# Kernel tuning notes

Measured on AMD Instinct MI355X. Metric: run time of the kernel, lower is better.

The kernel has to match this reference:

```python
import jax, jax.numpy as jnp
import numpy as np

K = 5            # kernel_size
MAX_ORIENT = 8
MAX_LEVEL = 4
D = (K - 1) // 2  # pad amount = 2


def setup_inputs() -> dict:
    key = jax.random.key(0)
    k1, k2, k3 = jax.random.split(key, 3)
    x = jax.random.normal(k1, (32, 1, 512, 512), dtype=jnp.float32)
    fwd_f = jax.random.normal(k2, (MAX_ORIENT, 1, K, K), dtype=jnp.float32)
    fwd_f = fwd_f.at[0, 0].set(jnp.ones((K, K), dtype=jnp.float32))  # per __init__
    inv_f = jax.random.normal(k3, (MAX_ORIENT, 1, K, K), dtype=jnp.float32)
    return {"x": x, "forward_filters": fwd_f, "inverse_filters": inv_f}


def _pad_for_tconv(p):
    # faithful port of padding_for_transpose_conv (static python ints)
    ip, op = 0, 0
    if p > 0:
        op = p
    elif p < 0:
        a = -p
        if a % 2 == 0:
            ip = a // 2
        else:
            op = 1
            ip = (a + 1) // 2
    return ip, op


def _conv2d(x, w, stride, pad):
    # torch F.pad(x, (d,d,d,d)) then conv2d(stride) == conv with symmetric padding
    return jax.lax.conv_general_dilated(
        x, w, window_strides=(stride, stride),
        padding=((pad, pad), (pad, pad)),
        dimension_numbers=("NCHW", "OIHW", "NCHW"))


def _conv_transpose2d(x, w, stride, pad, out_pad):
    # torch conv_transpose2d, weight layout (in_ch, out_ch, kH, kW).
    # Equivalent direct conv: flip kernel spatially, swap I/O axes,
    # lhs_dilation=stride, padding lo=k-1-p, hi=k-1-p+output_padding.
    k = w.shape[2]
    w2 = jnp.transpose(jnp.flip(w, (2, 3)), (1, 0, 2, 3))  # OIHW (1,8,5,5)
    padding = tuple((k - 1 - p, k - 1 - p + op) for p, op in zip(pad, out_pad))
    return jax.lax.conv_general_dilated(
        x, w2, window_strides=(1, 1), padding=padding,
        lhs_dilation=(stride, stride),
        dimension_numbers=("NCHW", "OIHW", "NCHW"))


def _forward_transform(x, fwd_f):
    result = [None] * (MAX_LEVEL + 1)
    vimg = x
    level = MAX_LEVEL
    res = None
    while level > 0 and vimg.shape[2] > 1 and vimg.shape[3] > 1:
        res = _conv2d(vimg, fwd_f, 2, D)   # (B, 8, ceil(H/2)+?, ...)
        result[level] = res
        vimg = res[:, :1]                  # lowpass band feeds next level
        level -= 1
    result[0] = res[:, :1]
    return result


def _inverse_transform(coeffs, inp_dim, inv_f):
    rec = coeffs[0]
    for level in range(1, MAX_LEVEL + 1):
        cur = np.array(coeffs[level].shape[2:])
        target = np.array(inp_dim) if level == MAX_LEVEL else np.array(coeffs[level + 1].shape[2:])
        pc = target - 2 * (cur - 1) - K
        ip0, op0 = _pad_for_tconv(int(pc[0]))
        ip1, op1 = _pad_for_tconv(int(pc[1]))
        full = jnp.concatenate([rec, coeffs[level][:, 1:]], axis=1)  # (B,8,h,w)
        rec = _conv_transpose2d(full, inv_f, 2, (ip0, ip1), (op0, op1))
    return rec


def reference(x, forward_filters, inverse_filters):
    coeffs = _forward_transform(x, forward_filters)
    return _inverse_transform(coeffs, x.shape[2:], inverse_filters)
```

## Files before the change

### kernel.cpp

```cpp
#include <hip/hip_runtime.h>

#define NORIENT 8

__device__ __forceinline__ unsigned xcd_swz(unsigned bid, unsigned nwg) {
    unsigned chunk = nwg >> 3;
    return (nwg & 7u) ? bid : (bid & 7u) * chunk + (bid >> 3);
}

__global__ void fwd_conv_wave_kernel(const float* __restrict__ in, long in_img_stride,
                                     const float* __restrict__ filt,
                                     float* __restrict__ out,
                                     int H, int W, int OH, int OW, int N) {
    constexpr int SROW = 104;
    __shared__ float tile[67 * SROW];

    int nbx = OW >> 5, nby = OH >> 5;
    unsigned sb = xcd_swz(blockIdx.x, gridDim.x);
    int bx = (int)(sb % nbx);
    unsigned t = sb / nbx;
    int by = (int)(t % nby);
    int n = (int)(t / nby);

    const float* __restrict__ ip = in + (long)n * in_img_stride;
    int tid = threadIdx.x;

    int w = __builtin_amdgcn_readfirstlane(tid >> 6);
    const float* __restrict__ F = filt + w * 25;
    float Wt[25];
#pragma unroll
    for (int k = 0; k < 25; ++k) Wt[k] = F[k];

    int gy0 = 64 * by - 2, gx0 = 64 * bx - 4;
#pragma unroll
    for (int k = 0; k < 3; ++k) {
        int e = tid + k * 512;
        if (e < 67 * 18) {
            int row = e / 18, m = e - row * 18;
            int gy = gy0 + row, gx = gx0 + 4 * m;
            bool vl = (gy >= 0) & (gy < H) & (gx >= 0) & (gx <= W - 4);
            float4 val = *(const float4*)(ip + (vl ? ((long)gy * W + gx) : 0));
            float msk = vl ? 1.f : 0.f;
            int off = row * SROW + 4 * m + 4 * (m >> 1);
            *(float4*)&tile[off] = make_float4(val.x * msk, val.y * msk,
                                               val.z * msk, val.w * msk);
        }
    }
    __syncthreads();

    int lane = tid & 63;
    int lx = lane & 7, ly = lane >> 3;

    float acc[4][4];
#pragma unroll
    for (int o = 0; o < 4; ++o)
#pragma unroll
        for (int dx = 0; dx < 4; ++dx) acc[o][dx] = 0.f;

#pragma unroll
    for (int r = 0; r < 11; ++r) {
        int base = (8 * ly + r) * SROW + 12 * lx;
        float4 A = *(const float4*)&tile[base];
        float4 B = *(const float4*)&tile[base + 4];
        float4 C = *(const float4*)&tile[base + 12];
        float4 Dd = *(const float4*)&tile[base + 16];
        float P[16] = {A.x, A.y, A.z, A.w, B.x, B.y, B.z, B.w,
                       C.x, C.y, C.z, C.w, Dd.x, Dd.y, Dd.z, Dd.w};

#pragma unroll
        for (int o = 0; o < 4; ++o) {
            int i = r - 2 * o;
            if (i < 0 || i > 4) continue;
#pragma unroll
            for (int j = 0; j < 5; ++j) {
                float wv = Wt[i * 5 + j];
#pragma unroll
                for (int dx = 0; dx < 4; ++dx)
                    acc[o][dx] = fmaf(P[2 + 2 * dx + j], wv, acc[o][dx]);
            }
        }
    }

    long cs = (long)OH * OW;
    int oy = 32 * by + 4 * ly, ox = 32 * bx + 4 * lx;
    long ob = ((long)n * NORIENT + w) * cs + (long)oy * OW + ox;
#pragma unroll
    for (int o = 0; o < 4; ++o)
        *(float4*)(out + ob + (long)o * OW) =
            make_float4(acc[o][0], acc[o][1], acc[o][2], acc[o][3]);
}

__global__ void inv_tconv_kernel(const float* __restrict__ rec, long rec_img_stride,
                                 const float* __restrict__ coef,
                                 const float* __restrict__ filt,
                                 float* __restrict__ out,
                                 int h, int w, int N) {
    int h2 = h >> 1, w2 = w >> 1;
    unsigned sb = xcd_swz(blockIdx.x, gridDim.x);
    long idx = (long)sb * blockDim.x + threadIdx.x;
    long total = (long)N * h2 * w2;
    if (idx >= total) return;
    int b0 = (int)(idx % w2);
    long t = idx / w2;
    int a0 = (int)(t % h2);
    int n = (int)(t / h2);

    const float* __restrict__ rp = rec + (long)n * rec_img_stride;
    const float* __restrict__ cp = coef + (long)n * (long)NORIENT * h * w;
    int cs = h * w;

    bool fmv = a0 > 0, fpv = a0 < h2 - 1;
    bool um = b0 > 0, up = b0 < w2 - 1;
    float fm = fmv ? 1.f : 0.f, fp_ = fpv ? 1.f : 0.f;
    int r0 = (fmv ? 2 * a0 - 1 : 0) * w;
    int r1 = (2 * a0) * w;
    int r2 = (2 * a0 + 1) * w;
    int r3 = (fpv ? 2 * a0 + 2 : 2 * a0 + 1) * w;
    int cL = um ? 2 * b0 - 2 : 0;
    int cM = 2 * b0;
    int cR = up ? 2 * b0 + 2 : 0;

    float acc[2][2][2][2];
#pragma unroll
    for (int i = 0; i < 2; ++i)
#pragma unroll
        for (int j = 0; j < 2; ++j)
#pragma unroll
            for (int k = 0; k < 2; ++k)
#pragma unroll
                for (int l = 0; l < 2; ++l) acc[i][j][k][l] = 0.f;

    auto do_channel = [&](const float* __restrict__ src, const float* __restrict__ F) {
        float P[4][4];
        const int ro[4] = {r0, r1, r2, r3};
        const float rm[4] = {fm, 1.f, 1.f, fp_};
#pragma unroll
        for (int r = 0; r < 4; ++r) {
            const float* base = src + ro[r];
            float2 L = *(const float2*)(base + cL);
            float2 M = *(const float2*)(base + cM);
            float2 R = *(const float2*)(base + cR);
            float mask = rm[r];
            P[r][0] = (um ? L.y : 0.f) * mask;
            P[r][1] = M.x * mask;
            P[r][2] = M.y * mask;
            P[r][3] = (up ? R.x : 0.f) * mask;
        }
#pragma unroll
        for (int a = 0; a < 3; ++a) {
#pragma unroll
            for (int b = 0; b < 3; ++b) {
                float w00 = F[(4 - 2 * a) * 5 + (4 - 2 * b)];
                float w01 = (b >= 1) ? F[(4 - 2 * a) * 5 + (5 - 2 * b)] : 0.f;
                float w10 = (a >= 1) ? F[(5 - 2 * a) * 5 + (4 - 2 * b)] : 0.f;
                float w11 = (a >= 1 && b >= 1) ? F[(5 - 2 * a) * 5 + (5 - 2 * b)] : 0.f;
#pragma unroll
                for (int sr = 0; sr < 2; ++sr) {
#pragma unroll
                    for (int sc = 0; sc < 2; ++sc) {
                        float pv = P[sr + a][sc + b];
                        acc[sr][sc][0][0] = fmaf(pv, w00, acc[sr][sc][0][0]);
                        if (b >= 1) acc[sr][sc][0][1] = fmaf(pv, w01, acc[sr][sc][0][1]);
                        if (a >= 1) acc[sr][sc][1][0] = fmaf(pv, w10, acc[sr][sc][1][0]);
                        if (a >= 1 && b >= 1)
                                    acc[sr][sc][1][1] = fmaf(pv, w11, acc[sr][sc][1][1]);
                    }
                }
            }
        }
    };

    do_channel(rp, filt);
#pragma unroll
    for (int c = 1; c < NORIENT; ++c)
        do_channel(cp + (long)c * cs, filt + c * 25);

    int OW = w << 1;
    long ob = (long)n * 4 * (long)cs + (long)(4 * a0) * OW + 4 * b0;
    *(float4*)(out + ob)          = make_float4(acc[0][0][0][0], acc[0][0][0][1],
                                                acc[0][1][0][0], acc[0][1][0][1]);
    *(float4*)(out + ob + OW)     = make_float4(acc[0][0][1][0], acc[0][0][1][1],
                                                acc[0][1][1][0], acc[0][1][1][1]);
    *(float4*)(out + ob + 2 * OW) = make_float4(acc[1][0][0][0], acc[1][0][0][1],
                                                acc[1][1][0][0], acc[1][1][0][1]);
    *(float4*)(out + ob + 3 * OW) = make_float4(acc[1][0][1][0], acc[1][0][1][1],
                                                acc[1][1][1][0], acc[1][1][1][1]);
}

extern "C" void kernel_launch(void* const* d_in, const int* in_sizes, int n_in,
                              void* d_out, int out_size, void* d_ws, size_t ws_size,
                              hipStream_t stream) {
    const float* x     = (const float*)d_in[0];
    const float* fwd_f = (const float*)d_in[1];
    const float* inv_f = (const float*)d_in[2];
    float* out = (float*)d_out;
    float* ws  = (float*)d_ws;

    const int N = 32;

    float* l4 = ws;
    float* l3 = l4 + 16777216;
    float* l2 = l3 + 4194304;
    float* l1 = l2 + 1048576;
    float* r1 = l1 + 262144;
    float* r2 = r1 + 131072;
    float* r3 = r2 + 524288;

    dim3 blkF(512), blk(256);
    auto nblocks = [](long total) { return dim3((unsigned)((total + 255) / 256)); };

    fwd_conv_wave_kernel<<<dim3(32 * 8 * 8), blkF, 0, stream>>>(
        x, 512L * 512, fwd_f, l4, 512, 512, 256, 256, N);
    fwd_conv_wave_kernel<<<dim3(32 * 4 * 4), blkF, 0, stream>>>(
        l4, 8L * 256 * 256, fwd_f, l3, 256, 256, 128, 128, N);
    fwd_conv_wave_kernel<<<dim3(32 * 2 * 2), blkF, 0, stream>>>(
        l3, 8L * 128 * 128, fwd_f, l2, 128, 128, 64, 64, N);
    fwd_conv_wave_kernel<<<dim3(32 * 1 * 1), blkF, 0, stream>>>(
        l2, 8L * 64 * 64, fwd_f, l1, 64, 64, 32, 32, N);

    inv_tconv_kernel<<<nblocks(32L * 16 * 16), blk, 0, stream>>>(
        l1, 8L * 32 * 32, l1, inv_f, r1, 32, 32, N);
    inv_tconv_kernel<<<nblocks(32L * 32 * 32), blk, 0, stream>>>(
        r1, 64L * 64, l2, inv_f, r2, 64, 64, N);
    inv_tconv_kernel<<<nblocks(32L * 64 * 64), blk, 0, stream>>>(
        r2, 128L * 128, l3, inv_f, r3, 128, 128, N);
    inv_tconv_kernel<<<nblocks(32L * 128 * 128), blk, 0, stream>>>(
        r3, 256L * 256, l4, inv_f, out, 256, 256, N);
}
```

Before: 96.53 us.

## Stage inverse transposed-conv input tiles in LDS for all eight channels

The inverse transposed-convolution kernel now assigns each 256-thread block a 32x32 input tile, loads a haloed 34x40 patch of all eight channel planes into shared memory with float4 loads, and computes from LDS. Previously each thread did overlapping global float2 loads with per-thread boundary logic. The aim is to remove redundant global and cache traffic and the masking arithmetic, at the cost of a large LDS footprint (about 43 KB per block), which may limit occupancy.

```diff
diff --git a/kernel.cpp b/kernel.cpp
--- a/kernel.cpp
+++ b/kernel.cpp
@@ -89,35 +89,78 @@
             make_float4(acc[o][0], acc[o][1], acc[o][2], acc[o][3]);
 }
 
-__global__ void inv_tconv_kernel(const float* __restrict__ rec, long rec_img_stride,
-                                 const float* __restrict__ coef,
-                                 const float* __restrict__ filt,
-                                 float* __restrict__ out,
-                                 int h, int w, int N) {
-    int h2 = h >> 1, w2 = w >> 1;
+__global__ void inv_tconv_lds_kernel(const float* __restrict__ rec, long rec_img_stride,
+                                     const float* __restrict__ coef,
+                                     const float* __restrict__ filt,
+                                     float* __restrict__ out,
+                                     int h, int w, int N) {
+    constexpr int SROW = 40;
+    constexpr int CH = 34 * SROW;
+    __shared__ float tile[NORIENT * CH];
+
+    int nbx = w >> 5, nby = h >> 5;
     unsigned sb = xcd_swz(blockIdx.x, gridDim.x);
-    long idx = (long)sb * blockDim.x + threadIdx.x;
-    long total = (long)N * h2 * w2;
-    if (idx >= total) return;
-    int b0 = (int)(idx % w2);
-    long t = idx / w2;
-    int a0 = (int)(t % h2);
-    int n = (int)(t / h2);
-
+    int bx = (int)(sb % nbx);
+    unsigned tt = sb / nbx;
+    int by = (int)(tt % nby);
+    int n = (int)(tt / nby);
+
+    int S0 = 32 * by, Q0 = 32 * bx;
+    long cs = (long)h * w;
     const float* __restrict__ rp = rec + (long)n * rec_img_stride;
-    const float* __restrict__ cp = coef + (long)n * (long)NORIENT * h * w;
-    int cs = h * w;
-
-    bool fmv = a0 > 0, fpv = a0 < h2 - 1;
-    bool um = b0 > 0, up = b0 < w2 - 1;
-    float fm = fmv ? 1.f : 0.f, fp_ = fpv ? 1.f : 0.f;
-    int r0 = (fmv ? 2 * a0 - 1 : 0) * w;
-    int r1 = (2 * a0) * w;
-    int r2 = (2 * a0 + 1) * w;
-    int r3 = (fpv ? 2 * a0 + 2 : 2 * a0 + 1) * w;
-    int cL = um ? 2 * b0 - 2 : 0;
-    int cM = 2 * b0;
-    int cR = up ? 2 * b0 + 2 : 0;
+    const float* __restrict__ cp = coef + (long)n * NORIENT * cs;
+
+    int tid = threadIdx.x;
+
+    {
+        float4 v[6]; int o[6]; unsigned msk = 0;
+#pragma unroll
+        for (int k = 0; k < 6; ++k) {
+            int e = tid + 256 * k;
+            int ech = e / 340, rem = e - ech * 340;
+            int row = rem / 10, m = rem - row * 10;
+            int gy = S0 - 1 + row, gx = Q0 - 4 + 4 * m;
+            bool vl = (gy >= 0) & (gy < h) & (gx >= 0) & (gx <= w - 4);
+            const float* __restrict__ src = ech ? (cp + (long)ech * cs) : rp;
+            v[k] = *(const float4*)(src + (vl ? ((long)gy * w + gx) : 0));
+            o[k] = ech * CH + row * SROW + 4 * m;
+            msk |= (vl ? 1u : 0u) << k;
+        }
+#pragma unroll
+        for (int k = 0; k < 6; ++k) {
+            float mm = ((msk >> k) & 1u) ? 1.f : 0.f;
+            *(float4*)&tile[o[k]] = make_float4(v[k].x * mm, v[k].y * mm,
+                                                v[k].z * mm, v[k].w * mm);
+        }
+    }
+    {
+        float4 v[5]; int o[5]; unsigned msk = 0;
+#pragma unroll
+        for (int k = 0; k < 5; ++k) {
+            int e = tid + 256 * (6 + k);
+            bool inr = e < 2720;
+            int e2 = inr ? e : 0;
+            int ech = e2 / 340, rem = e2 - ech * 340;
+            int row = rem / 10, m = rem - row * 10;
+            int gy = S0 - 1 + row, gx = Q0 - 4 + 4 * m;
+            bool vl = inr & (gy >= 0) & (gy < h) & (gx >= 0) & (gx <= w - 4);
+            const float* __restrict__ src = ech ? (cp + (long)ech * cs) : rp;
+            v[k] = *(const float4*)(src + (vl ? ((long)gy * w + gx) : 0));
+            o[k] = inr ? (ech * CH + row * SROW + 4 * m) : -1;
+            msk |= (vl ? 1u : 0u) << k;
+        }
+#pragma unroll
+        for (int k = 0; k < 5; ++k) {
+            if (o[k] >= 0) {
+                float mm = ((msk >> k) & 1u) ? 1.f : 0.f;
+                *(float4*)&tile[o[k]] = make_float4(v[k].x * mm, v[k].y * mm,
+                                                    v[k].z * mm, v[k].w * mm);
+            }
+        }
+    }
+    __syncthreads();
+
+    int sx = tid & 15, sy = tid >> 4;
 
     float acc[2][2][2][2];
 #pragma unroll
@@ -129,22 +172,20 @@
 #pragma unroll
                 for (int l = 0; l < 2; ++l) acc[i][j][k][l] = 0.f;
 
-    auto do_channel = [&](const float* __restrict__ src, const float* __restrict__ F) {
+#pragma unroll
+    for (int c = 0; c < NORIENT; ++c) {
+        const float* __restrict__ F = filt + c * 25;
+        const float* __restrict__ tc = &tile[c * CH];
+
         float P[4][4];
-        const int ro[4] = {r0, r1, r2, r3};
-        const float rm[4] = {fm, 1.f, 1.f, fp_};
 #pragma unroll
         for (int r = 0; r < 4; ++r) {
-            const float* base = src + ro[r];
-            float2 L = *(const float2*)(base + cL);
-            float2 M = *(const float2*)(base + cM);
-            float2 R = *(const float2*)(base + cR);
-            float mask = rm[r];
-            P[r][0] = (um ? L.y : 0.f) * mask;
-            P[r][1] = M.x * mask;
-            P[r][2] = M.y * mask;
-            P[r][3] = (up ? R.x : 0.f) * mask;
-        }
+            const float* rowp = tc + (2 * sy + r) * SROW;
+            float2 L = *(const float2*)(rowp + 2 * sx + 2);
+            float4 Ff = *(const float4*)(rowp + 2 * sx + 4);
+            P[r][0] = L.y; P[r][1] = Ff.x; P[r][2] = Ff.y; P[r][3] = Ff.z;
+        }
+
 #pragma unroll
         for (int a = 0; a < 3; ++a) {
 #pragma unroll
@@ -167,15 +208,10 @@
                 }
             }
         }
-    };
-
-    do_channel(rp, filt);
-#pragma unroll
-    for (int c = 1; c < NORIENT; ++c)
-        do_channel(cp + (long)c * cs, filt + c * 25);
+    }
 
     int OW = w << 1;
-    long ob = (long)n * 4 * (long)cs + (long)(4 * a0) * OW + 4 * b0;
+    long ob = (long)n * 4 * cs + (long)(2 * S0 + 4 * sy) * OW + (2 * Q0 + 4 * sx);
     *(float4*)(out + ob)          = make_float4(acc[0][0][0][0], acc[0][0][0][1],
                                                 acc[0][1][0][0], acc[0][1][0][1]);
     *(float4*)(out + ob + OW)     = make_float4(acc[0][0][1][0], acc[0][0][1][1],
@@ -206,7 +242,6 @@
     float* r3 = r2 + 524288;
 
     dim3 blkF(512), blk(256);
-    auto nblocks = [](long total) { return dim3((unsigned)((total + 255) / 256)); };
 
     fwd_conv_wave_kernel<<<dim3(32 * 8 * 8), blkF, 0, stream>>>(
         x, 512L * 512, fwd_f, l4, 512, 512, 256, 256, N);
@@ -217,12 +252,12 @@
     fwd_conv_wave_kernel<<<dim3(32 * 1 * 1), blkF, 0, stream>>>(
         l2, 8L * 64 * 64, fwd_f, l1, 64, 64, 32, 32, N);
 
-    inv_tconv_kernel<<<nblocks(32L * 16 * 16), blk, 0, stream>>>(
+    inv_tconv_lds_kernel<<<dim3(32 * 1 * 1), blk, 0, stream>>>(
         l1, 8L * 32 * 32, l1, inv_f, r1, 32, 32, N);
-    inv_tconv_kernel<<<nblocks(32L * 32 * 32), blk, 0, stream>>>(
+    inv_tconv_lds_kernel<<<dim3(32 * 2 * 2), blk, 0, stream>>>(
         r1, 64L * 64, l2, inv_f, r2, 64, 64, N);
-    inv_tconv_kernel<<<nblocks(32L * 64 * 64), blk, 0, stream>>>(
+    inv_tconv_lds_kernel<<<dim3(32 * 4 * 4), blk, 0, stream>>>(
         r2, 128L * 128, l3, inv_f, r3, 128, 128, N);
-    inv_tconv_kernel<<<nblocks(32L * 128 * 128), blk, 0, stream>>>(
+    inv_tconv_lds_kernel<<<dim3(32 * 8 * 8), blk, 0, stream>>>(
         r3, 256L * 256, l4, inv_f, out, 256, 256, N);
 }
```

Measured after the change: 110.9 us. +14.9%, slower.

## Split inverse transposed-conv channels across two thread halves with LDS reduction

Applied to the files above, without the earlier changes.

The inverse transposed-convolution kernel now runs 512 threads per block. Each output position is handled by two threads, each taking four of the eight channels, and their partial accumulators are summed through shared memory before the first half writes the result. This doubles the thread count for the small inverse levels, which were short of parallelism and latency-bound on the sequential channel loop. In exchange it adds an LDS buffer, a block barrier and extra reduction traffic, and the larger LDS footprint may lower occupancy on the biggest level.

```diff
diff --git a/kernel.cpp b/kernel.cpp
--- a/kernel.cpp
+++ b/kernel.cpp
@@ -89,16 +89,20 @@
             make_float4(acc[o][0], acc[o][1], acc[o][2], acc[o][3]);
 }
 
-__global__ void inv_tconv_kernel(const float* __restrict__ rec, long rec_img_stride,
-                                 const float* __restrict__ coef,
-                                 const float* __restrict__ filt,
-                                 float* __restrict__ out,
-                                 int h, int w, int N) {
+__global__ void inv_tconv_split_kernel(const float* __restrict__ rec, long rec_img_stride,
+                                       const float* __restrict__ coef,
+                                       const float* __restrict__ filt,
+                                       float* __restrict__ out,
+                                       int h, int w, int N) {
+    __shared__ float red[256 * 20];
+
     int h2 = h >> 1, w2 = w >> 1;
     unsigned sb = xcd_swz(blockIdx.x, gridDim.x);
-    long idx = (long)sb * blockDim.x + threadIdx.x;
-    long total = (long)N * h2 * w2;
-    if (idx >= total) return;
+    int tid = threadIdx.x;
+    int idx256 = tid & 255;
+    int half = tid >> 8;
+
+    long idx = (long)sb * 256 + idx256;
     int b0 = (int)(idx % w2);
     long t = idx / w2;
     int a0 = (int)(t % h2);
@@ -106,7 +110,7 @@
 
     const float* __restrict__ rp = rec + (long)n * rec_img_stride;
     const float* __restrict__ cp = coef + (long)n * (long)NORIENT * h * w;
-    int cs = h * w;
+    long cs = (long)h * w;
 
     bool fmv = a0 > 0, fpv = a0 < h2 - 1;
     bool um = b0 > 0, up = b0 < w2 - 1;
@@ -169,21 +173,47 @@
         }
     };
 
-    do_channel(rp, filt);
-#pragma unroll
-    for (int c = 1; c < NORIENT; ++c)
-        do_channel(cp + (long)c * cs, filt + c * 25);
-
-    int OW = w << 1;
-    long ob = (long)n * 4 * (long)cs + (long)(4 * a0) * OW + 4 * b0;
-    *(float4*)(out + ob)          = make_float4(acc[0][0][0][0], acc[0][0][0][1],
-                                                acc[0][1][0][0], acc[0][1][0][1]);
-    *(float4*)(out + ob + OW)     = make_float4(acc[0][0][1][0], acc[0][0][1][1],
-                                                acc[0][1][1][0], acc[0][1][1][1]);
-    *(float4*)(out + ob + 2 * OW) = make_float4(acc[1][0][0][0], acc[1][0][0][1],
-                                                acc[1][1][0][0], acc[1][1][0][1]);
-    *(float4*)(out + ob + 3 * OW) = make_float4(acc[1][0][1][0], acc[1][0][1][1],
-                                                acc[1][1][1][0], acc[1][1][1][1]);
+    if (half == 0) {
+        do_channel(rp, filt);
+#pragma unroll
+        for (int c = 1; c < 4; ++c)
+            do_channel(cp + (long)c * cs, filt + c * 25);
+    } else {
+#pragma unroll
+        for (int c = 4; c < 8; ++c)
+            do_channel(cp + (long)c * cs, filt + c * 25);
+    }
+
+    const float* a = &acc[0][0][0][0];
+    if (half == 1) {
+#pragma unroll
+        for (int k = 0; k < 4; ++k)
+            *(float4*)&red[idx256 * 20 + 4 * k] =
+                make_float4(a[4 * k], a[4 * k + 1], a[4 * k + 2], a[4 * k + 3]);
+    }
+    __syncthreads();
+    if (half == 0) {
+        float* aw = &acc[0][0][0][0];
+#pragma unroll
+        for (int k = 0; k < 4; ++k) {
+            float4 r = *(const float4*)&red[idx256 * 20 + 4 * k];
+            aw[4 * k]     += r.x;
+            aw[4 * k + 1] += r.y;
+            aw[4 * k + 2] += r.z;
+            aw[4 * k + 3] += r.w;
+        }
+
+        int OW = w << 1;
+        long ob = (long)n * 4 * cs + (long)(4 * a0) * OW + 4 * b0;
+        *(float4*)(out + ob)          = make_float4(acc[0][0][0][0], acc[0][0][0][1],
+                                                    acc[0][1][0][0], acc[0][1][0][1]);
+        *(float4*)(out + ob + OW)     = make_float4(acc[0][0][1][0], acc[0][0][1][1],
+                                                    acc[0][1][1][0], acc[0][1][1][1]);
+        *(float4*)(out + ob + 2 * OW) = make_float4(acc[1][0][0][0], acc[1][0][0][1],
+                                                    acc[1][1][0][0], acc[1][1][0][1]);
+        *(float4*)(out + ob + 3 * OW) = make_float4(acc[1][0][1][0], acc[1][0][1][1],
+                                                    acc[1][1][1][0], acc[1][1][1][1]);
+    }
 }
 
 extern "C" void kernel_launch(void* const* d_in, const int* in_sizes, int n_in,
@@ -205,8 +235,7 @@
     float* r2 = r1 + 131072;
     float* r3 = r2 + 524288;
 
-    dim3 blkF(512), blk(256);
-    auto nblocks = [](long total) { return dim3((unsigned)((total + 255) / 256)); };
+    dim3 blkF(512), blkI(512);
 
     fwd_conv_wave_kernel<<<dim3(32 * 8 * 8), blkF, 0, stream>>>(
         x, 512L * 512, fwd_f, l4, 512, 512, 256, 256, N);
@@ -217,12 +246,12 @@
     fwd_conv_wave_kernel<<<dim3(32 * 1 * 1), blkF, 0, stream>>>(
         l2, 8L * 64 * 64, fwd_f, l1, 64, 64, 32, 32, N);
 
-    inv_tconv_kernel<<<nblocks(32L * 16 * 16), blk, 0, stream>>>(
+    inv_tconv_split_kernel<<<dim3(32), blkI, 0, stream>>>(
         l1, 8L * 32 * 32, l1, inv_f, r1, 32, 32, N);
-    inv_tconv_kernel<<<nblocks(32L * 32 * 32), blk, 0, stream>>>(
+    inv_tconv_split_kernel<<<dim3(128), blkI, 0, stream>>>(
         r1, 64L * 64, l2, inv_f, r2, 64, 64, N);
-    inv_tconv_kernel<<<nblocks(32L * 64 * 64), blk, 0, stream>>>(
+    inv_tconv_split_kernel<<<dim3(512), blkI, 0, stream>>>(
         r2, 128L * 128, l3, inv_f, r3, 128, 128, N);
-    inv_tconv_kernel<<<nblocks(32L * 128 * 128), blk, 0, stream>>>(
+    inv_tconv_split_kernel<<<dim3(2048), blkI, 0, stream>>>(
         r3, 256L * 256, l4, inv_f, out, 256, 256, N);
 }
```

Result: no change. 98.43 us (+2.0%).

## Store level-4 highpass coefficients in bf16 and split lowpass to separate buffer

Applied to the files above, without the earlier changes.

The first forward level now writes its lowpass channel as fp32 into a compact buffer and the seven highpass channels as bf16 into a separate buffer. The next forward level reads the compact lowpass buffer, and the last inverse level reads the bf16 highpass bands, converting them back to fp32. This halves the traffic for the largest intermediate, which is written once and read once, in what is a memory-bound pipeline. The cost is reduced precision in the highpass coefficients, which may exceed the output tolerance.

```diff
diff --git a/kernel.cpp b/kernel.cpp
--- a/kernel.cpp
+++ b/kernel.cpp
@@ -5,6 +5,108 @@
 __device__ __forceinline__ unsigned xcd_swz(unsigned bid, unsigned nwg) {
     unsigned chunk = nwg >> 3;
     return (nwg & 7u) ? bid : (bid & 7u) * chunk + (bid >> 3);
+}
+
+__device__ __forceinline__ float bf2f(unsigned short u) {
+    return __uint_as_float((unsigned)u << 16);
+}
+__device__ __forceinline__ unsigned short f2bf(float f) {
+    unsigned b = __float_as_uint(f);
+    return (unsigned short)((b + 0x7FFFu + ((b >> 16) & 1u)) >> 16);
+}
+
+__global__ void fwd_conv_wave_l1_kernel(const float* __restrict__ in, long in_img_stride,
+                                        const float* __restrict__ filt,
+                                        float* __restrict__ outc0,
+                                        unsigned short* __restrict__ outb,
+                                        int H, int W, int OH, int OW, int N) {
+    constexpr int SROW = 104;
+    __shared__ float tile[67 * SROW];
+
+    int nbx = OW >> 5, nby = OH >> 5;
+    unsigned sb = xcd_swz(blockIdx.x, gridDim.x);
+    int bx = (int)(sb % nbx);
+    unsigned t = sb / nbx;
+    int by = (int)(t % nby);
+    int n = (int)(t / nby);
+
+    const float* __restrict__ ip = in + (long)n * in_img_stride;
+    int tid = threadIdx.x;
+
+    int w = __builtin_amdgcn_readfirstlane(tid >> 6);
+    const float* __restrict__ F = filt + w * 25;
+    float Wt[25];
+#pragma unroll
+    for (int k = 0; k < 25; ++k) Wt[k] = F[k];
+
+    int gy0 = 64 * by - 2, gx0 = 64 * bx - 4;
+#pragma unroll
+    for (int k = 0; k < 3; ++k) {
+        int e = tid + k * 512;
+        if (e < 67 * 18) {
+            int row = e / 18, m = e - row * 18;
+            int gy = gy0 + row, gx = gx0 + 4 * m;
+            bool vl = (gy >= 0) & (gy < H) & (gx >= 0) & (gx <= W - 4);
+            float4 val = *(const float4*)(ip + (vl ? ((long)gy * W + gx) : 0));
+            float msk = vl ? 1.f : 0.f;
+            int off = row * SROW + 4 * m + 4 * (m >> 1);
+            *(float4*)&tile[off] = make_float4(val.x * msk, val.y * msk,
+                                               val.z * msk, val.w * msk);
+        }
+    }
+    __syncthreads();
+
+    int lane = tid & 63;
+    int lx = lane & 7, ly = lane >> 3;
+
+    float acc[4][4];
+#pragma unroll
+    for (int o = 0; o < 4; ++o)
+#pragma unroll
+        for (int dx = 0; dx < 4; ++dx) acc[o][dx] = 0.f;
+
+#pragma unroll
+    for (int r = 0; r < 11; ++r) {
+        int base = (8 * ly + r) * SROW + 12 * lx;
+        float4 A = *(const float4*)&tile[base];
+        float4 B = *(const float4*)&tile[base + 4];
+        float4 C = *(const float4*)&tile[base + 12];
+        float4 Dd = *(const float4*)&tile[base + 16];
+        float P[16] = {A.x, A.y, A.z, A.w, B.x, B.y, B.z, B.w,
+                       C.x, C.y, C.z, C.w, Dd.x, Dd.y, Dd.z, Dd.w};
+
+#pragma unroll
+        for (int o = 0; o < 4; ++o) {
+            int i = r - 2 * o;
+            if (i < 0 || i > 4) continue;
+#pragma unroll
+            for (int j = 0; j < 5; ++j) {
+                float wv = Wt[i * 5 + j];
+#pragma unroll
+                for (int dx = 0; dx < 4; ++dx)
+                    acc[o][dx] = fmaf(P[2 + 2 * dx + j], wv, acc[o][dx]);
+            }
+        }
+    }
+
+    long cs = (long)OH * OW;
+    int oy = 32 * by + 4 * ly, ox = 32 * bx + 4 * lx;
+    if (w == 0) {
+        long ob = (long)n * cs + (long)oy * OW + ox;
+#pragma unroll
+        for (int o = 0; o < 4; ++o)
+            *(float4*)(outc0 + ob + (long)o * OW) =
+                make_float4(acc[o][0], acc[o][1], acc[o][2], acc[o][3]);
+    } else {
+        long ob = ((long)n * 7 + (w - 1)) * cs + (long)oy * OW + ox;
+#pragma unroll
+        for (int o = 0; o < 4; ++o) {
+            ushort4 u;
+            u.x = f2bf(acc[o][0]); u.y = f2bf(acc[o][1]);
+            u.z = f2bf(acc[o][2]); u.w = f2bf(acc[o][3]);
+            *(ushort4*)(outb + ob + (long)o * OW) = u;
+        }
+    }
 }
 
 __global__ void fwd_conv_wave_kernel(const float* __restrict__ in, long in_img_stride,
@@ -106,7 +208,7 @@
 
     const float* __restrict__ rp = rec + (long)n * rec_img_stride;
     const float* __restrict__ cp = coef + (long)n * (long)NORIENT * h * w;
-    int cs = h * w;
+    long cs = (long)h * w;
 
     bool fmv = a0 > 0, fpv = a0 < h2 - 1;
     bool um = b0 > 0, up = b0 < w2 - 1;
@@ -175,7 +277,7 @@
         do_channel(cp + (long)c * cs, filt + c * 25);
 
     int OW = w << 1;
-    long ob = (long)n * 4 * (long)cs + (long)(4 * a0) * OW + 4 * b0;
+    long ob = (long)n * 4 * cs + (long)(4 * a0) * OW + 4 * b0;
     *(float4*)(out + ob)          = make_float4(acc[0][0][0][0], acc[0][0][0][1],
                                                 acc[0][1][0][0], acc[0][1][0][1]);
     *(float4*)(out + ob + OW)     = make_float4(acc[0][0][1][0], acc[0][0][1][1],
@@ -186,6 +288,122 @@
                                                 acc[1][1][1][0], acc[1][1][1][1]);
 }
 
+__global__ void inv_tconv_bf16_kernel(const float* __restrict__ rec, long rec_img_stride,
+                                      const unsigned short* __restrict__ coefb,
+                                      const float* __restrict__ filt,
+                                      float* __restrict__ out,
+                                      int h, int w, int N) {
+    int h2 = h >> 1, w2 = w >> 1;
+    unsigned sb = xcd_swz(blockIdx.x, gridDim.x);
+    long idx = (long)sb * blockDim.x + threadIdx.x;
+    long total = (long)N * h2 * w2;
+    if (idx >= total) return;
+    int b0 = (int)(idx % w2);
+    long t = idx / w2;
+    int a0 = (int)(t % h2);
+    int n = (int)(t / h2);
+
+    const float* __restrict__ rp = rec + (long)n * rec_img_stride;
+    long cs = (long)h * w;
+    const unsigned short* __restrict__ cpb = coefb + (long)n * 7 * cs;
+
+    bool fmv = a0 > 0, fpv = a0 < h2 - 1;
+    bool um = b0 > 0, up = b0 < w2 - 1;
+    float fm = fmv ? 1.f : 0.f, fp_ = fpv ? 1.f : 0.f;
+    int r0 = (fmv ? 2 * a0 - 1 : 0) * w;
+    int r1 = (2 * a0) * w;
+    int r2 = (2 * a0 + 1) * w;
+    int r3 = (fpv ? 2 * a0 + 2 : 2 * a0 + 1) * w;
+    int cL = um ? 2 * b0 - 2 : 0;
+    int cM = 2 * b0;
+    int cR = up ? 2 * b0 + 2 : 0;
+
+    const int ro[4] = {r0, r1, r2, r3};
+    const float rm[4] = {fm, 1.f, 1.f, fp_};
+
+    float acc[2][2][2][2];
+#pragma unroll
+    for (int i = 0; i < 2; ++i)
+#pragma unroll
+        for (int j = 0; j < 2; ++j)
+#pragma unroll
+            for (int k = 0; k < 2; ++k)
+#pragma unroll
+                for (int l = 0; l < 2; ++l) acc[i][j][k][l] = 0.f;
+
+    auto accum = [&](const float P[4][4], const float* __restrict__ F) {
+#pragma unroll
+        for (int a = 0; a < 3; ++a) {
+#pragma unroll
+            for (int b = 0; b < 3; ++b) {
+                float w00 = F[(4 - 2 * a) * 5 + (4 - 2 * b)];
+                float w01 = (b >= 1) ? F[(4 - 2 * a) * 5 + (5 - 2 * b)] : 0.f;
+                float w10 = (a >= 1) ? F[(5 - 2 * a) * 5 + (4 - 2 * b)] : 0.f;
+                float w11 = (a >= 1 && b >= 1) ? F[(5 - 2 * a) * 5 + (5 - 2 * b)] : 0.f;
+#pragma unroll
+                for (int sr = 0; sr < 2; ++sr) {
+#pragma unroll
+                    for (int sc = 0; sc < 2; ++sc) {
+                        float pv = P[sr + a][sc + b];
+                        acc[sr][sc][0][0] = fmaf(pv, w00, acc[sr][sc][0][0]);
+                        if (b >= 1) acc[sr][sc][0][1] = fmaf(pv, w01, acc[sr][sc][0][1]);
+                        if (a >= 1) acc[sr][sc][1][0] = fmaf(pv, w10, acc[sr][sc][1][0]);
+                        if (a >= 1 && b >= 1)
+                                    acc[sr][sc][1][1] = fmaf(pv, w11, acc[sr][sc][1][1]);
+                    }
+                }
+            }
+        }
+    };
+
+    {
+        float P[4][4];
+#pragma unroll
+        for (int r = 0; r < 4; ++r) {
+            const float* base = rp + ro[r];
+            float2 L = *(const float2*)(base + cL);
+            float2 M = *(const float2*)(base + cM);
+            float2 R = *(const float2*)(base + cR);
+            float mask = rm[r];
+            P[r][0] = (um ? L.y : 0.f) * mask;
+            P[r][1] = M.x * mask;
+            P[r][2] = M.y * mask;
+            P[r][3] = (up ? R.x : 0.f) * mask;
+        }
+        accum(P, filt);
+    }
+
+#pragma unroll
+    for (int c = 1; c < NORIENT; ++c) {
+        const unsigned short* __restrict__ src = cpb + (long)(c - 1) * cs;
+        float P[4][4];
+#pragma unroll
+        for (int r = 0; r < 4; ++r) {
+            const unsigned short* base = src + ro[r];
+            ushort2 L = *(const ushort2*)(base + cL);
+            ushort2 M = *(const ushort2*)(base + cM);
+            ushort2 R = *(const ushort2*)(base + cR);
+            float mask = rm[r];
+            P[r][0] = (um ? bf2f(L.y) : 0.f) * mask;
+            P[r][1] = bf2f(M.x) * mask;
+            P[r][2] = bf2f(M.y) * mask;
+            P[r][3] = (up ? bf2f(R.x) : 0.f) * mask;
+        }
+        accum(P, filt + c * 25);
+    }
+
+    int OW = w << 1;
+    long ob = (long)n * 4 * cs + (long)(4 * a0) * OW + 4 * b0;
+    *(float4*)(out + ob)          = make_float4(acc[0][0][0][0], acc[0][0][0][1],
+                                                acc[0][1][0][0], acc[0][1][0][1]);
+    *(float4*)(out + ob + OW)     = make_float4(acc[0][0][1][0], acc[0][0][1][1],
+                                                acc[0][1][1][0], acc[0][1][1][1]);
+    *(float4*)(out + ob + 2 * OW) = make_float4(acc[1][0][0][0], acc[1][0][0][1],
+                                                acc[1][1][0][0], acc[1][1][0][1]);
+    *(float4*)(out + ob + 3 * OW) = make_float4(acc[1][0][1][0], acc[1][0][1][1],
+                                                acc[1][1][1][0], acc[1][1][1][1]);
+}
+
 extern "C" void kernel_launch(void* const* d_in, const int* in_sizes, int n_in,
                               void* d_out, int out_size, void* d_ws, size_t ws_size,
                               hipStream_t stream) {
@@ -197,8 +415,9 @@
 
     const int N = 32;
 
-    float* l4 = ws;
-    float* l3 = l4 + 16777216;
+    float* l4c0 = ws;
+    unsigned short* l4b = (unsigned short*)(ws + 2097152);
+    float* l3 = ws + 2097152 + 7340032;
     float* l2 = l3 + 4194304;
     float* l1 = l2 + 1048576;
     float* r1 = l1 + 262144;
@@ -208,10 +427,10 @@
     dim3 blkF(512), blk(256);
     auto nblocks = [](long total) { return dim3((unsigned)((total + 255) / 256)); };
 
-    fwd_conv_wave_kernel<<<dim3(32 * 8 * 8), blkF, 0, stream>>>(
-        x, 512L * 512, fwd_f, l4, 512, 512, 256, 256, N);
+    fwd_conv_wave_l1_kernel<<<dim3(32 * 8 * 8), blkF, 0, stream>>>(
+        x, 512L * 512, fwd_f, l4c0, l4b, 512, 512, 256, 256, N);
     fwd_conv_wave_kernel<<<dim3(32 * 4 * 4), blkF, 0, stream>>>(
-        l4, 8L * 256 * 256, fwd_f, l3, 256, 256, 128, 128, N);
+        l4c0, 65536L, fwd_f, l3, 256, 256, 128, 128, N);
     fwd_conv_wave_kernel<<<dim3(32 * 2 * 2), blkF, 0, stream>>>(
         l3, 8L * 128 * 128, fwd_f, l2, 128, 128, 64, 64, N);
     fwd_conv_wave_kernel<<<dim3(32 * 1 * 1), blkF, 0, stream>>>(
@@ -223,6 +442,6 @@
         r1, 64L * 64, l2, inv_f, r2, 64, 64, N);
     inv_tconv_kernel<<<nblocks(32L * 64 * 64), blk, 0, stream>>>(
         r2, 128L * 128, l3, inv_f, r3, 128, 128, N);
-    inv_tconv_kernel<<<nblocks(32L * 128 * 128), blk, 0, stream>>>(
-        r3, 256L * 256, l4, inv_f, out, 256, 256, N);
-}
+    inv_tconv_bf16_kernel<<<nblocks(32L * 128 * 128), blk, 0, stream>>>(
+        r3, 256L * 256, l4b, inv_f, out, 256, 256, N);
+}
```

New measurement: 106.4 us. 10.2% more time.
